# Kernel optimization log

Measured on AMD Instinct MI355X. Metric: run time of the kernel, lower is better.

The kernel has to match this reference:

```python
import jax, jax.numpy as jnp
import numpy as np

B, N, E = 8, 50000, 400000
DIMS = [4, 64, 64, 3]
K = 3
EPS = 1e-5
NEG_SLOPE = 0.01


def _gcn_norm(edge_index, num_nodes):
    # TAGConv uses gcn_norm with unit edge weights and add_self_loops=False.
    row, col = edge_index[0], edge_index[1]
    w = jnp.ones(row.shape[0], dtype=jnp.float32)
    deg = jax.ops.segment_sum(w, col, num_segments=num_nodes)  # in-degree at target
    dis = jnp.where(deg > 0, jnp.power(jnp.maximum(deg, 1.0), -0.5), 0.0)
    return dis[row] * dis[col]  # [E]


def _tag_conv(x, W, b, row, col, norm, num_nodes):
    # x: [B, N, Fin]; W: [K+1, Fin, Fout]; b: [Fout]
    out = jnp.einsum('bnf,fg->bng', x, W[0])
    h = x
    for k in range(1, W.shape[0]):
        msg = h[:, row, :] * norm[None, :, None]            # [B, E, Fin] gather
        h = jnp.zeros((x.shape[0], num_nodes, x.shape[2]), x.dtype).at[:, col, :].add(msg)  # scatter-add
        out = out + jnp.einsum('bnf,fg->bng', h, W[k])
    return out + b


def _batchnorm(x2d, gamma, beta):
    # training-mode BatchNorm1d over batch dim (biased variance, eps=1e-5)
    mean = jnp.mean(x2d, axis=0)
    var = jnp.mean(jnp.square(x2d - mean), axis=0)
    return gamma * (x2d - mean) * jax.lax.rsqrt(var + EPS) + beta


def _leaky_relu(x):
    return jnp.where(x >= 0, x, NEG_SLOPE * x)


def setup_inputs() -> dict:
    key = jax.random.key(0)
    ks = jax.random.split(key, 12)
    inp = {}
    inp['x'] = jax.random.normal(ks[0], (B, N, DIMS[0]), dtype=jnp.float32)
    inp['edge_index'] = jax.random.randint(ks[1], (2, E), 0, N, dtype=jnp.int64)
    inp['val_min'] = jax.random.uniform(ks[2], (N, 3), dtype=jnp.float32) - 1.5
    inp['val_max'] = jax.random.uniform(ks[3], (N, 3), dtype=jnp.float32) + 0.5
    for l in range(3):
        fin, fout = DIMS[l], DIMS[l + 1]
        scale = 1.0 / np.sqrt(fin)
        inp[f'W{l}'] = jax.random.uniform(ks[4 + l], (K + 1, fin, fout), minval=-scale, maxval=scale, dtype=jnp.float32)
        inp[f'b{l}'] = jnp.zeros((fout,), jnp.float32)
    for l in range(2):
        inp[f'gamma{l}'] = jnp.ones((N * DIMS[l + 1],), jnp.float32)
        inp[f'beta{l}'] = jnp.zeros((N * DIMS[l + 1],), jnp.float32)
    return inp


def reference(x, edge_index, val_min, val_max, W0, b0, W1, b1, W2, b2,
              gamma0, beta0, gamma1, beta1):
    row, col = edge_index[0], edge_index[1]
    norm = _gcn_norm(edge_index, N)
    Ws = [W0, W1, W2]
    bs = [b0, b1, b2]
    gammas = [gamma0, gamma1]
    betas = [beta0, beta1]
    out = x
    for layer in range(2):  # num_layers - 1 hidden layers
        out = _tag_conv(out, Ws[layer], bs[layer], row, col, norm, N)
        d = DIMS[layer + 1]
        out = _batchnorm(out.reshape(-1, N * d), gammas[layer], betas[layer]).reshape(-1, N, d)
        out = _leaky_relu(out)
    out = _tag_conv(out, Ws[2], bs[2], row, col, norm, N)  # [B, N, 3]
    # non_linearity: gamma = min + (max - min) / (1 + exp(U))
    return val_min[None] + (val_max - val_min)[None] / (1.0 + jnp.exp(out))
```

## Files before the change

kernel.cpp:

```cpp
#include <hip/hip_runtime.h>
#include <math.h>

constexpr int B = 8;
constexpr int N = 50000;
constexpr int E = 400000;
constexpr float BN_EPS = 1e-5f;
constexpr float NEG = 0.01f;


__device__ __forceinline__ unsigned clamp_src(int s) {
    unsigned u = (unsigned)s;
    return (u < (unsigned)N) ? u : 0u;
}

__device__ __forceinline__ unsigned pack_bf16(float a, float b) {
    unsigned ua = __float_as_uint(a);
    unsigned ub = __float_as_uint(b);
    ua = (ua + 0x7FFFu + ((ua >> 16) & 1u)) >> 16;
    ub = (ub + 0x7FFFu + ((ub >> 16) & 1u)) >> 16;
    return (ub << 16) | (ua & 0xFFFFu);
}
__device__ __forceinline__ float unpack_lo(unsigned u) { return __uint_as_float(u << 16); }
__device__ __forceinline__ float unpack_hi(unsigned u) { return __uint_as_float(u & 0xFFFF0000u); }

__device__ __forceinline__ void store_row64_f32(float* p, const float acc[64]) {
#pragma unroll
    for (int q = 0; q < 16; ++q)
        *(float4*)(p + q * 4) = make_float4(acc[q * 4], acc[q * 4 + 1], acc[q * 4 + 2], acc[q * 4 + 3]);
}
__device__ __forceinline__ void store_row64_bf(void* op, const float acc[64]) {
    uint4* p = (uint4*)op;
#pragma unroll
    for (int q = 0; q < 8; ++q) {
        uint4 v;
        v.x = pack_bf16(acc[q * 8 + 0], acc[q * 8 + 1]);
        v.y = pack_bf16(acc[q * 8 + 2], acc[q * 8 + 3]);
        v.z = pack_bf16(acc[q * 8 + 4], acc[q * 8 + 5]);
        v.w = pack_bf16(acc[q * 8 + 6], acc[q * 8 + 7]);
        p[q] = v;
    }
}


__global__ __launch_bounds__(256) void deg_kernel(const int* __restrict__ col, float* __restrict__ deg) {
    int e = blockIdx.x * blockDim.x + threadIdx.x;
    if (e < E) atomicAdd(&deg[clamp_src(col[e])], 1.0f);
}

__global__ __launch_bounds__(256) void scan1_kernel(const float* __restrict__ deg,
                                                    int* __restrict__ part, int* __restrict__ bsum) {
    __shared__ int sm[4];
    int i = blockIdx.x * blockDim.x + threadIdx.x;
    int v = (i < N) ? (int)deg[i] : 0;
    int lane = threadIdx.x & 63, wv = threadIdx.x >> 6;
    int x = v;
#pragma unroll
    for (int off = 1; off < 64; off <<= 1) {
        int t = __shfl_up(x, off);
        if (lane >= off) x += t;
    }
    if (lane == 63) sm[wv] = x;
    __syncthreads();
    int add = 0;
#pragma unroll
    for (int w = 0; w < 4; ++w) if (w < wv) add += sm[w];
    if (i < N) part[i] = x - v + add;
    if (threadIdx.x == blockDim.x - 1) bsum[blockIdx.x] = x + add;
}

__global__ __launch_bounds__(256) void scan2_kernel(const int* __restrict__ bsum, int* __restrict__ boff,
                                                    int nb, int* __restrict__ rowptr) {
    __shared__ int sm[4];
    int i = threadIdx.x;
    int v = (i < nb) ? bsum[i] : 0;
    int lane = i & 63, wv = i >> 6;
    int x = v;
#pragma unroll
    for (int off = 1; off < 64; off <<= 1) {
        int t = __shfl_up(x, off);
        if (lane >= off) x += t;
    }
    if (lane == 63) sm[wv] = x;
    __syncthreads();
    int add = 0;
#pragma unroll
    for (int w = 0; w < 4; ++w) if (w < wv) add += sm[w];
    if (i < nb) boff[i] = x - v + add;
    if (i == 0) rowptr[N] = E;
}

__global__ __launch_bounds__(256) void scan3_kernel(const int* __restrict__ part, const int* __restrict__ boff,
                                                    int* __restrict__ rowptr) {
    int i = blockIdx.x * blockDim.x + threadIdx.x;
    if (i < N) rowptr[i] = part[i] + boff[blockIdx.x];
}

__global__ __launch_bounds__(256) void fill_kernel(const int* __restrict__ row, const int* __restrict__ col,
                                                   const float* __restrict__ deg, const int* __restrict__ rowptr,
                                                   int* __restrict__ cursor, int* __restrict__ csr_src,
                                                   float* __restrict__ csr_w) {
    int e = blockIdx.x * blockDim.x + threadIdx.x;
    if (e >= E) return;
    unsigned r = clamp_src(row[e]), c = clamp_src(col[e]);
    float dr = deg[r], dc = deg[c];
    float w = (dr > 0.f ? rsqrtf(dr) : 0.f) * (dc > 0.f ? rsqrtf(dc) : 0.f);
    unsigned p = (unsigned)(rowptr[c] + atomicAdd(&cursor[c], 1));
    if (p >= (unsigned)E) p = E - 1;
    csr_src[p] = (int)r;
    csr_w[p] = w;
}


template<bool INBF>
__global__ __launch_bounds__(256) void xprop_kernel(const void* __restrict__ xin, const int* __restrict__ rowptr,
                                                    const int* __restrict__ csr_src, const float* __restrict__ csr_w,
                                                    uint2* __restrict__ xout) {
    int b = blockIdx.x & 7;
    int nb = blockIdx.x >> 3;
    int n = nb * blockDim.x + threadIdx.x;
    if (n >= N) return;
    float a0 = 0.f, a1 = 0.f, a2 = 0.f, a3 = 0.f;
    int beg = rowptr[n], end = rowptr[n + 1];
    if (beg < 0) beg = 0;
    if (end > E) end = E;
    for (int i = beg; i < end; ++i) {
        unsigned s = clamp_src(csr_src[i]);
        float w = csr_w[i];
        if constexpr (!INBF) {
            float4 v = *((const float4*)xin + (size_t)b * N + s);
            a0 = fmaf(w, v.x, a0); a1 = fmaf(w, v.y, a1);
            a2 = fmaf(w, v.z, a2); a3 = fmaf(w, v.w, a3);
        } else {
            uint2 v = *((const uint2*)xin + (size_t)b * N + s);
            a0 = fmaf(w, unpack_lo(v.x), a0); a1 = fmaf(w, unpack_hi(v.x), a1);
            a2 = fmaf(w, unpack_lo(v.y), a2); a3 = fmaf(w, unpack_hi(v.y), a3);
        }
    }
    uint2 o;
    o.x = pack_bf16(a0, a1);
    o.y = pack_bf16(a2, a3);
    xout[(size_t)b * N + n] = o;
}


__global__ __launch_bounds__(256) void fused0_kernel(const float* __restrict__ x0, const uint2* __restrict__ x1,
                                                     const uint2* __restrict__ x2, const uint2* __restrict__ x3,
                                                     const float* __restrict__ W0, const float* __restrict__ bias,
                                                     const float* __restrict__ gamma, const float* __restrict__ beta,
                                                     void* __restrict__ h1) {
    int gid = blockIdx.x * blockDim.x + threadIdx.x;
    int wave = gid >> 6, lane = gid & 63;
    int n = wave * 8 + (lane >> 3);
    int b = lane & 7;
    if (n >= N) return;
    size_t ro = (size_t)b * N + n;
    float xv[16];
    {
        float4 v = *((const float4*)x0 + ro);
        xv[0] = v.x; xv[1] = v.y; xv[2] = v.z; xv[3] = v.w;
        uint2 u1 = x1[ro], u2 = x2[ro], u3 = x3[ro];
        xv[4] = unpack_lo(u1.x); xv[5] = unpack_hi(u1.x); xv[6] = unpack_lo(u1.y); xv[7] = unpack_hi(u1.y);
        xv[8] = unpack_lo(u2.x); xv[9] = unpack_hi(u2.x); xv[10] = unpack_lo(u2.y); xv[11] = unpack_hi(u2.y);
        xv[12] = unpack_lo(u3.x); xv[13] = unpack_hi(u3.x); xv[14] = unpack_lo(u3.y); xv[15] = unpack_hi(u3.y);
    }
    float acc[64];
#pragma unroll
    for (int f = 0; f < 64; ++f) acc[f] = bias[f];
#pragma unroll
    for (int kf = 0; kf < 16; ++kf) {
        float xs = xv[kf];
#pragma unroll
        for (int f = 0; f < 64; ++f)
            acc[f] = fmaf(xs, W0[kf * 64 + f], acc[f]);
    }
    const float* gp = gamma + (size_t)n * 64;
    const float* bp = beta + (size_t)n * 64;
#pragma unroll
    for (int f = 0; f < 64; ++f) {
        float v = acc[f];
        float s = v, s2 = v * v;
        s += __shfl_xor(s, 1);  s += __shfl_xor(s, 2);  s += __shfl_xor(s, 4);
        s2 += __shfl_xor(s2, 1); s2 += __shfl_xor(s2, 2); s2 += __shfl_xor(s2, 4);
        float mean = s * 0.125f;
        float var = fmaf(-mean, mean, s2 * 0.125f);
        float xn = (v - mean) * rsqrtf(var + BN_EPS);
        float o = fmaf(gp[f], xn, bp[f]);
        acc[f] = (o >= 0.f) ? o : NEG * o;
    }
    store_row64_bf((char*)h1 + ro * 128, acc);
}


__device__ __forceinline__ void dense64_bf(const uint4* __restrict__ hp8, const float* __restrict__ W, float acc[64]) {
#pragma unroll 1
    for (int kk = 0; kk < 4; ++kk) {
        float hreg[16];
        uint4 va = hp8[kk * 2], vb = hp8[kk * 2 + 1];
        hreg[0] = unpack_lo(va.x); hreg[1] = unpack_hi(va.x);
        hreg[2] = unpack_lo(va.y); hreg[3] = unpack_hi(va.y);
        hreg[4] = unpack_lo(va.z); hreg[5] = unpack_hi(va.z);
        hreg[6] = unpack_lo(va.w); hreg[7] = unpack_hi(va.w);
        hreg[8] = unpack_lo(vb.x); hreg[9] = unpack_hi(vb.x);
        hreg[10] = unpack_lo(vb.y); hreg[11] = unpack_hi(vb.y);
        hreg[12] = unpack_lo(vb.z); hreg[13] = unpack_hi(vb.z);
        hreg[14] = unpack_lo(vb.w); hreg[15] = unpack_hi(vb.w);
        const float* Wp = W + kk * 16 * 64;
#pragma unroll
        for (int k = 0; k < 16; ++k) {
            float hv = hreg[k];
#pragma unroll
            for (int c = 0; c < 64; ++c)
                acc[c] = fmaf(hv, Wp[k * 64 + c], acc[c]);
        }
    }
}

__device__ __forceinline__ void gather64_f32(const float* __restrict__ ub, int beg, int end,
                                             const int* __restrict__ csr_src, const float* __restrict__ csr_w,
                                             float acc[64]) {
    if (beg < 0) beg = 0;
    if (end > E) end = E;
    for (int i = beg; i < end; ++i) {
        unsigned s = clamp_src(csr_src[i]);
        float w = csr_w[i];
        const float4* up = (const float4*)(ub + (size_t)s * 64);
#pragma unroll
        for (int q = 0; q < 16; ++q) {
            float4 v = up[q];
            acc[q * 4 + 0] = fmaf(w, v.x, acc[q * 4 + 0]);
            acc[q * 4 + 1] = fmaf(w, v.y, acc[q * 4 + 1]);
            acc[q * 4 + 2] = fmaf(w, v.z, acc[q * 4 + 2]);
            acc[q * 4 + 3] = fmaf(w, v.w, acc[q * 4 + 3]);
        }
    }
}

__device__ __forceinline__ void gather64_bf(const char* __restrict__ ub, int beg, int end,
                                            const int* __restrict__ csr_src, const float* __restrict__ csr_w,
                                            float acc[64]) {
    if (beg < 0) beg = 0;
    if (end > E) end = E;
    for (int i = beg; i < end; ++i) {
        unsigned s = clamp_src(csr_src[i]);
        float w = csr_w[i];
        const uint4* up = (const uint4*)(ub + (size_t)s * 128);
#pragma unroll
        for (int q = 0; q < 8; ++q) {
            uint4 v = up[q];
            acc[q * 8 + 0] = fmaf(w, unpack_lo(v.x), acc[q * 8 + 0]);
            acc[q * 8 + 1] = fmaf(w, unpack_hi(v.x), acc[q * 8 + 1]);
            acc[q * 8 + 2] = fmaf(w, unpack_lo(v.y), acc[q * 8 + 2]);
            acc[q * 8 + 3] = fmaf(w, unpack_hi(v.y), acc[q * 8 + 3]);
            acc[q * 8 + 4] = fmaf(w, unpack_lo(v.z), acc[q * 8 + 4]);
            acc[q * 8 + 5] = fmaf(w, unpack_hi(v.z), acc[q * 8 + 5]);
            acc[q * 8 + 6] = fmaf(w, unpack_lo(v.w), acc[q * 8 + 6]);
            acc[q * 8 + 7] = fmaf(w, unpack_hi(v.w), acc[q * 8 + 7]);
        }
    }
}


template<bool OUTBF>
__global__ __launch_bounds__(64) void hop_kernel(const float* __restrict__ u_in, const int* __restrict__ rowptr,
                                                 const int* __restrict__ csr_src, const float* __restrict__ csr_w,
                                                 const uint4* __restrict__ h1, int b0, int bshift, int bmask,
                                                 const float* __restrict__ W, void* __restrict__ out) {
    int bl = blockIdx.x & bmask;
    int n = (blockIdx.x >> bshift) * blockDim.x + threadIdx.x;
    if (n >= N) return;
    int gb = b0 + bl;
    float acc[64];
#pragma unroll
    for (int f = 0; f < 64; ++f) acc[f] = 0.f;
    if (u_in)
        gather64_f32(u_in + (size_t)bl * N * 64, rowptr[n], rowptr[n + 1], csr_src, csr_w, acc);
    dense64_bf(h1 + ((size_t)gb * N + n) * 8, W, acc);
    if constexpr (OUTBF)
        store_row64_bf((char*)out + ((size_t)gb * N + n) * 128, acc);
    else
        store_row64_f32((float*)out + ((size_t)bl * N + n) * 64, acc);
}


template<bool UBF>
__global__ __launch_bounds__(256) void hop64_final_kernel(const void* __restrict__ u_in, const int* __restrict__ rowptr,
                                                          const int* __restrict__ csr_src, const float* __restrict__ csr_w,
                                                          const uint4* __restrict__ h1, const float* __restrict__ W,
                                                          const float* __restrict__ bias,
                                                          const float* __restrict__ gamma, const float* __restrict__ beta,
                                                          const float* __restrict__ W2, float* __restrict__ y) {
    int gid = blockIdx.x * blockDim.x + threadIdx.x;
    int wave = gid >> 6, lane = gid & 63;
    int n = wave * 8 + (lane >> 3);
    int b = lane & 7;
    if (n >= N) return;
    float acc[64];
#pragma unroll
    for (int f = 0; f < 64; ++f) acc[f] = bias[f];
    int beg = rowptr[n], end = rowptr[n + 1];
    if constexpr (UBF)
        gather64_bf((const char*)u_in + (size_t)b * N * 128, beg, end, csr_src, csr_w, acc);
    else
        gather64_f32((const float*)u_in + (size_t)b * N * 64, beg, end, csr_src, csr_w, acc);
    dense64_bf(h1 + ((size_t)b * N + n) * 8, W, acc);
    const float* gp = gamma + (size_t)n * 64;
    const float* bp = beta + (size_t)n * 64;
#pragma unroll
    for (int f = 0; f < 64; ++f) {
        float v = acc[f];
        float s = v, s2 = v * v;
        s += __shfl_xor(s, 1);  s += __shfl_xor(s, 2);  s += __shfl_xor(s, 4);
        s2 += __shfl_xor(s2, 1); s2 += __shfl_xor(s2, 2); s2 += __shfl_xor(s2, 4);
        float mean = s * 0.125f;
        float var = fmaf(-mean, mean, s2 * 0.125f);
        float xn = (v - mean) * rsqrtf(var + BN_EPS);
        float o = fmaf(gp[f], xn, bp[f]);
        acc[f] = (o >= 0.f) ? o : NEG * o;
    }
    size_t bn3 = ((size_t)b * N + n) * 3;
#pragma unroll
    for (int k = 0; k < 4; ++k) {
#pragma unroll
        for (int c = 0; c < 3; ++c) {
            float s = 0.f;
#pragma unroll
            for (int f = 0; f < 64; ++f)
                s = fmaf(acc[f], W2[k * 192 + f * 3 + c], s);
            y[(size_t)k * B * N * 3 + bn3 + c] = s;
        }
    }
}


__global__ __launch_bounds__(256) void qprop_kernel(const float* __restrict__ vin, const int* __restrict__ rowptr,
                                                    const int* __restrict__ csr_src, const float* __restrict__ csr_w,
                                                    const float* __restrict__ add, float* __restrict__ vout) {
    int b = blockIdx.x & 7;
    int nb = blockIdx.x >> 3;
    int n = nb * blockDim.x + threadIdx.x;
    if (n >= N) return;
    float a0 = 0.f, a1 = 0.f, a2 = 0.f;
    int beg = rowptr[n], end = rowptr[n + 1];
    if (beg < 0) beg = 0;
    if (end > E) end = E;
    const float* base = vin + (size_t)b * N * 3;
    for (int i = beg; i < end; ++i) {
        unsigned s = clamp_src(csr_src[i]);
        float w = csr_w[i];
        const float* p = base + (size_t)s * 3;
        a0 = fmaf(w, p[0], a0);
        a1 = fmaf(w, p[1], a1);
        a2 = fmaf(w, p[2], a2);
    }
    const float* ap = add + ((size_t)b * N + n) * 3;
    float* op = vout + ((size_t)b * N + n) * 3;
    op[0] = a0 + ap[0];
    op[1] = a1 + ap[1];
    op[2] = a2 + ap[2];
}

__global__ __launch_bounds__(256) void qfinal_kernel(const float* __restrict__ vin, const int* __restrict__ rowptr,
                                                     const int* __restrict__ csr_src, const float* __restrict__ csr_w,
                                                     const float* __restrict__ y0, const float* __restrict__ b2,
                                                     const float* __restrict__ vmin, const float* __restrict__ vmax,
                                                     float* __restrict__ out) {
    int b = blockIdx.x & 7;
    int nb = blockIdx.x >> 3;
    int n = nb * blockDim.x + threadIdx.x;
    if (n >= N) return;
    float a0 = 0.f, a1 = 0.f, a2 = 0.f;
    int beg = rowptr[n], end = rowptr[n + 1];
    if (beg < 0) beg = 0;
    if (end > E) end = E;
    const float* base = vin + (size_t)b * N * 3;
    for (int i = beg; i < end; ++i) {
        unsigned s = clamp_src(csr_src[i]);
        float w = csr_w[i];
        const float* p = base + (size_t)s * 3;
        a0 = fmaf(w, p[0], a0);
        a1 = fmaf(w, p[1], a1);
        a2 = fmaf(w, p[2], a2);
    }
    size_t bn3 = ((size_t)b * N + n) * 3;
    const float* yp = y0 + bn3;
    float g0 = a0 + yp[0] + b2[0];
    float g1 = a1 + yp[1] + b2[1];
    float g2 = a2 + yp[2] + b2[2];
    float mn0 = vmin[n * 3 + 0], mx0 = vmax[n * 3 + 0];
    float mn1 = vmin[n * 3 + 1], mx1 = vmax[n * 3 + 1];
    float mn2 = vmin[n * 3 + 2], mx2 = vmax[n * 3 + 2];
    float* op = out + bn3;
    op[0] = mn0 + (mx0 - mn0) / (1.f + expf(g0));
    op[1] = mn1 + (mx1 - mn1) / (1.f + expf(g1));
    op[2] = mn2 + (mx2 - mn2) / (1.f + expf(g2));
}


extern "C" void kernel_launch(void* const* d_in, const int* in_sizes, int n_in,
                              void* d_out, int out_size, void* d_ws, size_t ws_size,
                              hipStream_t stream) {
    const float* x      = (const float*)d_in[0];
    const int*   ei     = (const int*)d_in[1];
    const int*   rowi   = ei;
    const int*   coli   = ei + E;
    const float* vmin   = (const float*)d_in[2];
    const float* vmax   = (const float*)d_in[3];
    const float* W0     = (const float*)d_in[4];
    const float* b0v    = (const float*)d_in[5];
    const float* W1     = (const float*)d_in[6];
    const float* b1v    = (const float*)d_in[7];
    const float* W2     = (const float*)d_in[8];
    const float* b2v    = (const float*)d_in[9];
    const float* gamma0 = (const float*)d_in[10];
    const float* beta0  = (const float*)d_in[11];
    const float* gamma1 = (const float*)d_in[12];
    const float* beta1  = (const float*)d_in[13];
    float* out = (float*)d_out;

    const size_t PC   = (size_t)N * 64;
    const size_t BN3  = (size_t)B * N * 3;
    const size_t H1FL = (size_t)B * N * 32;
    const size_t XBFL = (size_t)B * N * 2;
    const size_t avail_fl = ws_size / 4;

    auto rnd = [](size_t nf) { return (nf + 63) & ~(size_t)63; };
    const size_t csr_fl = rnd(N) + rnd(E) + rnd(N + 1) + rnd(N) + 256 + 256 + rnd(N) + rnd(E);

    int cc;
    size_t yv_fl = rnd(4 * BN3) + 2 * rnd(BN3);
    auto shared_need = [&](int c) { return (size_t)2 * c * PC > yv_fl ? (size_t)2 * c * PC : yv_fl; };
    auto tot_chunked = [&](int c) { return csr_fl + H1FL + H1FL + shared_need(c); };
    size_t tot_full = csr_fl + H1FL + 2 * 8 * PC;
    if (avail_fl >= tot_full + (1 << 20))      cc = 8;
    else if (avail_fl >= tot_chunked(4) + (1 << 20)) cc = 4;
    else if (avail_fl >= tot_chunked(2) + (1 << 20)) cc = 2;
    else cc = 1;

    size_t off = 0;
    auto alloc = [&](size_t nfloats) -> float* {
        float* p = (float*)d_ws + off;
        off += rnd(nfloats);
        return p;
    };
    float* deg     = alloc(N);
    float* csr_w   = alloc(E);
    int*   rowptr  = (int*)alloc(N + 1);
    int*   part    = (int*)alloc(N);
    int*   bsum    = (int*)alloc(256);
    int*   boff    = (int*)alloc(256);
    int*   cursor  = (int*)alloc(N);
    int*   csr_src = (int*)alloc(E);
    float* h1      = alloc(H1FL);

    float *u_a, *u_b, *u2full = nullptr, *shared;
    uint2 *xb1, *xb2, *xb3;
    float *y, *v_a, *v_b;
    if (cc == 8) {
        u_a = alloc(8 * PC);
        u_b = alloc(8 * PC);
        xb1 = (uint2*)u_b; xb2 = (uint2*)(u_b + XBFL); xb3 = (uint2*)(u_b + 2 * XBFL);
        y = u_b; v_a = u_b + rnd(4 * BN3); v_b = v_a + rnd(BN3);
    } else {
        u2full = alloc(H1FL);
        shared = alloc(shared_need(cc));
        u_a = shared; u_b = shared + (size_t)cc * PC;
        xb1 = (uint2*)shared; xb2 = (uint2*)(shared + XBFL); xb3 = (uint2*)(shared + 2 * XBFL);
        y = shared; v_a = shared + rnd(4 * BN3); v_b = v_a + rnd(BN3);
    }

    const int GE = (E + 255) / 256;
    const int GN = (N + 255) / 256;
    const int GT = (B * N + 255) / 256;
    const int GH = (N + 63) / 64;
    dim3 blk(256);
    int bshift = (cc == 8) ? 3 : (cc == 4) ? 2 : (cc == 2) ? 1 : 0;
    int bmask = cc - 1;

    hipMemsetAsync(deg, 0, N * sizeof(float), stream);
    hipMemsetAsync(cursor, 0, N * sizeof(int), stream);
    deg_kernel<<<GE, blk, 0, stream>>>(coli, deg);
    scan1_kernel<<<GN, blk, 0, stream>>>(deg, part, bsum);
    scan2_kernel<<<1, blk, 0, stream>>>(bsum, boff, GN, rowptr);
    scan3_kernel<<<GN, blk, 0, stream>>>(part, boff, rowptr);
    fill_kernel<<<GE, blk, 0, stream>>>(rowi, coli, deg, rowptr, cursor, csr_src, csr_w);

    xprop_kernel<false><<<GN * 8, blk, 0, stream>>>(x,   rowptr, csr_src, csr_w, xb1);
    xprop_kernel<true><<<GN * 8, blk, 0, stream>>>(xb1, rowptr, csr_src, csr_w, xb2);
    xprop_kernel<true><<<GN * 8, blk, 0, stream>>>(xb2, rowptr, csr_src, csr_w, xb3);
    fused0_kernel<<<GT, blk, 0, stream>>>(x, xb1, xb2, xb3, W0, b0v, gamma0, beta0, h1);

    if (cc == 8) {
        hop_kernel<false><<<GH * 8, dim3(64), 0, stream>>>(nullptr, rowptr, csr_src, csr_w,
                                                           (const uint4*)h1, 0, 3, 7, W1 + 3 * 4096, u_a);
        hop_kernel<false><<<GH * 8, dim3(64), 0, stream>>>(u_a, rowptr, csr_src, csr_w,
                                                           (const uint4*)h1, 0, 3, 7, W1 + 2 * 4096, u_b);
        hop_kernel<false><<<GH * 8, dim3(64), 0, stream>>>(u_b, rowptr, csr_src, csr_w,
                                                           (const uint4*)h1, 0, 3, 7, W1 + 1 * 4096, u_a);
        hop64_final_kernel<false><<<GT, blk, 0, stream>>>(u_a, rowptr, csr_src, csr_w,
                                                          (const uint4*)h1, W1, b1v, gamma1, beta1, W2, y);
    } else {
        for (int b0 = 0; b0 < B; b0 += cc) {
            hop_kernel<false><<<GH * cc, dim3(64), 0, stream>>>(nullptr, rowptr, csr_src, csr_w,
                                                                (const uint4*)h1, b0, bshift, bmask,
                                                                W1 + 3 * 4096, u_a);
            hop_kernel<false><<<GH * cc, dim3(64), 0, stream>>>(u_a, rowptr, csr_src, csr_w,
                                                                (const uint4*)h1, b0, bshift, bmask,
                                                                W1 + 2 * 4096, u_b);
            hop_kernel<true><<<GH * cc, dim3(64), 0, stream>>>(u_b, rowptr, csr_src, csr_w,
                                                               (const uint4*)h1, b0, bshift, bmask,
                                                               W1 + 1 * 4096, u2full);
        }
        hop64_final_kernel<true><<<GT, blk, 0, stream>>>(u2full, rowptr, csr_src, csr_w,
                                                         (const uint4*)h1, W1, b1v, gamma1, beta1, W2, y);
    }

    qprop_kernel<<<GN * 8, blk, 0, stream>>>(y + 3 * BN3, rowptr, csr_src, csr_w, y + 2 * BN3, v_a);
    qprop_kernel<<<GN * 8, blk, 0, stream>>>(v_a, rowptr, csr_src, csr_w, y + 1 * BN3, v_b);
    qfinal_kernel<<<GN * 8, blk, 0, stream>>>(v_b, rowptr, csr_src, csr_w, y, b2v, vmin, vmax, out);
}
```

Measured before the change: 1.105 ms.

## Recompute layer-0 activations inside hop kernels instead of materializing h1

Layer 0 is split into a stats kernel that stores per-feature BatchNorm scale and shift (packed bf16) and no longer writes h1. Each layer-1 hop kernel recomputes h1 on the fly from the propagated inputs, W0 and the scale/shift, and then applies Wk. Hop intermediates become bf16 with 256-thread blocks, and the chunked memory-fallback paths are removed. This trades extra ALU work (a 16x64 recompute in each of four hops) for less memory traffic and bf16 gathers. Dropping b0 from the pre-BatchNorm value is exact, since training-mode BN removes the mean. Storing u in bf16 and scale/shift in bf16 lowers precision.

```diff
diff --git a/kernel.cpp b/kernel.cpp
--- a/kernel.cpp
+++ b/kernel.cpp
@@ -23,13 +23,7 @@
 __device__ __forceinline__ float unpack_lo(unsigned u) { return __uint_as_float(u << 16); }
 __device__ __forceinline__ float unpack_hi(unsigned u) { return __uint_as_float(u & 0xFFFF0000u); }
 
-__device__ __forceinline__ void store_row64_f32(float* p, const float acc[64]) {
-#pragma unroll
-    for (int q = 0; q < 16; ++q)
-        *(float4*)(p + q * 4) = make_float4(acc[q * 4], acc[q * 4 + 1], acc[q * 4 + 2], acc[q * 4 + 3]);
-}
-__device__ __forceinline__ void store_row64_bf(void* op, const float acc[64]) {
-    uint4* p = (uint4*)op;
+__device__ __forceinline__ void store_row64_bf(uint4* p, const float acc[64]) {
 #pragma unroll
     for (int q = 0; q < 8; ++q) {
         uint4 v;
@@ -116,8 +110,7 @@
                                                     const int* __restrict__ csr_src, const float* __restrict__ csr_w,
                                                     uint2* __restrict__ xout) {
     int b = blockIdx.x & 7;
-    int nb = blockIdx.x >> 3;
-    int n = nb * blockDim.x + threadIdx.x;
+    int n = (blockIdx.x >> 3) * blockDim.x + threadIdx.x;
     if (n >= N) return;
     float a0 = 0.f, a1 = 0.f, a2 = 0.f, a3 = 0.f;
     int beg = rowptr[n], end = rowptr[n + 1];
@@ -143,11 +136,23 @@
 }
 
 
-__global__ __launch_bounds__(256) void fused0_kernel(const float* __restrict__ x0, const uint2* __restrict__ x1,
-                                                     const uint2* __restrict__ x2, const uint2* __restrict__ x3,
-                                                     const float* __restrict__ W0, const float* __restrict__ bias,
-                                                     const float* __restrict__ gamma, const float* __restrict__ beta,
-                                                     void* __restrict__ h1) {
+__device__ __forceinline__ void load_xv(const float4* __restrict__ x0, const uint2* __restrict__ x1,
+                                        const uint2* __restrict__ x2, const uint2* __restrict__ x3,
+                                        size_t ro, float xv[16]) {
+    float4 v = x0[ro];
+    xv[0] = v.x; xv[1] = v.y; xv[2] = v.z; xv[3] = v.w;
+    uint2 u1 = x1[ro], u2 = x2[ro], u3 = x3[ro];
+    xv[4] = unpack_lo(u1.x); xv[5] = unpack_hi(u1.x); xv[6] = unpack_lo(u1.y); xv[7] = unpack_hi(u1.y);
+    xv[8] = unpack_lo(u2.x); xv[9] = unpack_hi(u2.x); xv[10] = unpack_lo(u2.y); xv[11] = unpack_hi(u2.y);
+    xv[12] = unpack_lo(u3.x); xv[13] = unpack_hi(u3.x); xv[14] = unpack_lo(u3.y); xv[15] = unpack_hi(u3.y);
+}
+
+
+__global__ __launch_bounds__(256) void stats_kernel(const float4* __restrict__ x0, const uint2* __restrict__ x1,
+                                                    const uint2* __restrict__ x2, const uint2* __restrict__ x3,
+                                                    const float* __restrict__ W0,
+                                                    const float* __restrict__ gamma, const float* __restrict__ beta,
+                                                    unsigned* __restrict__ ss) {
     int gid = blockIdx.x * blockDim.x + threadIdx.x;
     int wave = gid >> 6, lane = gid & 63;
     int n = wave * 8 + (lane >> 3);
@@ -155,87 +160,36 @@
     if (n >= N) return;
     size_t ro = (size_t)b * N + n;
     float xv[16];
-    {
-        float4 v = *((const float4*)x0 + ro);
-        xv[0] = v.x; xv[1] = v.y; xv[2] = v.z; xv[3] = v.w;
-        uint2 u1 = x1[ro], u2 = x2[ro], u3 = x3[ro];
-        xv[4] = unpack_lo(u1.x); xv[5] = unpack_hi(u1.x); xv[6] = unpack_lo(u1.y); xv[7] = unpack_hi(u1.y);
-        xv[8] = unpack_lo(u2.x); xv[9] = unpack_hi(u2.x); xv[10] = unpack_lo(u2.y); xv[11] = unpack_hi(u2.y);
-        xv[12] = unpack_lo(u3.x); xv[13] = unpack_hi(u3.x); xv[14] = unpack_lo(u3.y); xv[15] = unpack_hi(u3.y);
-    }
-    float acc[64];
-#pragma unroll
-    for (int f = 0; f < 64; ++f) acc[f] = bias[f];
+    load_xv(x0, x1, x2, x3, ro, xv);
+    float z[64];
+#pragma unroll
+    for (int f = 0; f < 64; ++f) z[f] = 0.f;
 #pragma unroll
     for (int kf = 0; kf < 16; ++kf) {
         float xs = xv[kf];
 #pragma unroll
         for (int f = 0; f < 64; ++f)
-            acc[f] = fmaf(xs, W0[kf * 64 + f], acc[f]);
+            z[f] = fmaf(xs, W0[kf * 64 + f], z[f]);
     }
     const float* gp = gamma + (size_t)n * 64;
     const float* bp = beta + (size_t)n * 64;
 #pragma unroll
     for (int f = 0; f < 64; ++f) {
-        float v = acc[f];
+        float v = z[f];
         float s = v, s2 = v * v;
         s += __shfl_xor(s, 1);  s += __shfl_xor(s, 2);  s += __shfl_xor(s, 4);
         s2 += __shfl_xor(s2, 1); s2 += __shfl_xor(s2, 2); s2 += __shfl_xor(s2, 4);
         float mean = s * 0.125f;
         float var = fmaf(-mean, mean, s2 * 0.125f);
-        float xn = (v - mean) * rsqrtf(var + BN_EPS);
-        float o = fmaf(gp[f], xn, bp[f]);
-        acc[f] = (o >= 0.f) ? o : NEG * o;
-    }
-    store_row64_bf((char*)h1 + ro * 128, acc);
-}
-
-
-__device__ __forceinline__ void dense64_bf(const uint4* __restrict__ hp8, const float* __restrict__ W, float acc[64]) {
-#pragma unroll 1
-    for (int kk = 0; kk < 4; ++kk) {
-        float hreg[16];
-        uint4 va = hp8[kk * 2], vb = hp8[kk * 2 + 1];
-        hreg[0] = unpack_lo(va.x); hreg[1] = unpack_hi(va.x);
-        hreg[2] = unpack_lo(va.y); hreg[3] = unpack_hi(va.y);
-        hreg[4] = unpack_lo(va.z); hreg[5] = unpack_hi(va.z);
-        hreg[6] = unpack_lo(va.w); hreg[7] = unpack_hi(va.w);
-        hreg[8] = unpack_lo(vb.x); hreg[9] = unpack_hi(vb.x);
-        hreg[10] = unpack_lo(vb.y); hreg[11] = unpack_hi(vb.y);
-        hreg[12] = unpack_lo(vb.z); hreg[13] = unpack_hi(vb.z);
-        hreg[14] = unpack_lo(vb.w); hreg[15] = unpack_hi(vb.w);
-        const float* Wp = W + kk * 16 * 64;
-#pragma unroll
-        for (int k = 0; k < 16; ++k) {
-            float hv = hreg[k];
-#pragma unroll
-            for (int c = 0; c < 64; ++c)
-                acc[c] = fmaf(hv, Wp[k * 64 + c], acc[c]);
-        }
-    }
-}
-
-__device__ __forceinline__ void gather64_f32(const float* __restrict__ ub, int beg, int end,
-                                             const int* __restrict__ csr_src, const float* __restrict__ csr_w,
-                                             float acc[64]) {
-    if (beg < 0) beg = 0;
-    if (end > E) end = E;
-    for (int i = beg; i < end; ++i) {
-        unsigned s = clamp_src(csr_src[i]);
-        float w = csr_w[i];
-        const float4* up = (const float4*)(ub + (size_t)s * 64);
-#pragma unroll
-        for (int q = 0; q < 16; ++q) {
-            float4 v = up[q];
-            acc[q * 4 + 0] = fmaf(w, v.x, acc[q * 4 + 0]);
-            acc[q * 4 + 1] = fmaf(w, v.y, acc[q * 4 + 1]);
-            acc[q * 4 + 2] = fmaf(w, v.z, acc[q * 4 + 2]);
-            acc[q * 4 + 3] = fmaf(w, v.w, acc[q * 4 + 3]);
-        }
-    }
-}
-
-__device__ __forceinline__ void gather64_bf(const char* __restrict__ ub, int beg, int end,
+        float rs = rsqrtf(var + BN_EPS);
+        float sc = gp[f] * rs;
+        float sh = fmaf(-sc, mean, bp[f]);
+        if (b == 0) ss[(size_t)n * 64 + f] = pack_bf16(sc, sh);
+    }
+}
+
+
+__device__ __forceinline__ void gather64_bf(const uint4* __restrict__ ub8, int beg, int end,
                                             const int* __restrict__ csr_src, const float* __restrict__ csr_w,
                                             float acc[64]) {
     if (beg < 0) beg = 0;
@@ -243,7 +197,7 @@
     for (int i = beg; i < end; ++i) {
         unsigned s = clamp_src(csr_src[i]);
         float w = csr_w[i];
-        const uint4* up = (const uint4*)(ub + (size_t)s * 128);
+        const uint4* up = ub8 + (size_t)s * 8;
 #pragma unroll
         for (int q = 0; q < 8; ++q) {
             uint4 v = up[q];
@@ -260,49 +214,72 @@
 }
 
 
-template<bool OUTBF>
-__global__ __launch_bounds__(64) void hop_kernel(const float* __restrict__ u_in, const int* __restrict__ rowptr,
-                                                 const int* __restrict__ csr_src, const float* __restrict__ csr_w,
-                                                 const uint4* __restrict__ h1, int b0, int bshift, int bmask,
-                                                 const float* __restrict__ W, void* __restrict__ out) {
-    int bl = blockIdx.x & bmask;
-    int n = (blockIdx.x >> bshift) * blockDim.x + threadIdx.x;
-    if (n >= N) return;
-    int gb = b0 + bl;
+template<int MODE>
+__global__ __launch_bounds__(256) void hopR_kernel(const uint4* __restrict__ u_in, const int* __restrict__ rowptr,
+                                                   const int* __restrict__ csr_src, const float* __restrict__ csr_w,
+                                                   const float4* __restrict__ x0, const uint2* __restrict__ x1,
+                                                   const uint2* __restrict__ x2, const uint2* __restrict__ x3,
+                                                   const float* __restrict__ W0, const unsigned* __restrict__ ss,
+                                                   const float* __restrict__ Wk, const float* __restrict__ bias,
+                                                   uint4* __restrict__ u_out) {
+    int b = blockIdx.x & 7;
+    int n = (blockIdx.x >> 3) * blockDim.x + threadIdx.x;
+    if (n >= N) return;
+    size_t ro = (size_t)b * N + n;
+    float xv[16];
+    load_xv(x0, x1, x2, x3, ro, xv);
     float acc[64];
-#pragma unroll
-    for (int f = 0; f < 64; ++f) acc[f] = 0.f;
-    if (u_in)
-        gather64_f32(u_in + (size_t)bl * N * 64, rowptr[n], rowptr[n + 1], csr_src, csr_w, acc);
-    dense64_bf(h1 + ((size_t)gb * N + n) * 8, W, acc);
-    if constexpr (OUTBF)
-        store_row64_bf((char*)out + ((size_t)gb * N + n) * 128, acc);
-    else
-        store_row64_f32((float*)out + ((size_t)bl * N + n) * 64, acc);
-}
-
-
-template<bool UBF>
-__global__ __launch_bounds__(256) void hop64_final_kernel(const void* __restrict__ u_in, const int* __restrict__ rowptr,
-                                                          const int* __restrict__ csr_src, const float* __restrict__ csr_w,
-                                                          const uint4* __restrict__ h1, const float* __restrict__ W,
-                                                          const float* __restrict__ bias,
-                                                          const float* __restrict__ gamma, const float* __restrict__ beta,
-                                                          const float* __restrict__ W2, float* __restrict__ y) {
+    if constexpr (MODE == 2) {
+#pragma unroll
+        for (int f = 0; f < 64; ++f) acc[f] = bias[f];
+    } else {
+#pragma unroll
+        for (int f = 0; f < 64; ++f) acc[f] = 0.f;
+    }
+    if constexpr (MODE > 0)
+        gather64_bf(u_in + (size_t)b * N * 8, rowptr[n], rowptr[n + 1], csr_src, csr_w, acc);
+    const unsigned* ssp = ss + (size_t)n * 64;
+#pragma unroll 1
+    for (int kq = 0; kq < 16; ++kq) {
+        uint4 sq = *(const uint4*)(ssp + kq * 4);
+        unsigned sqa[4] = {sq.x, sq.y, sq.z, sq.w};
+#pragma unroll
+        for (int j = 0; j < 4; ++j) {
+            int k = kq * 4 + j;
+            float z = 0.f;
+#pragma unroll
+            for (int kf = 0; kf < 16; ++kf)
+                z = fmaf(xv[kf], W0[kf * 64 + k], z);
+            float h = fmaf(z, unpack_lo(sqa[j]), unpack_hi(sqa[j]));
+            h = (h >= 0.f) ? h : NEG * h;
+            const float* wr = Wk + k * 64;
+#pragma unroll
+            for (int c = 0; c < 64; ++c)
+                acc[c] = fmaf(h, wr[c], acc[c]);
+        }
+    }
+    store_row64_bf(u_out + ro * 8, acc);
+}
+
+
+__global__ __launch_bounds__(256) void bn_project_kernel(const uint4* __restrict__ z,
+                                                         const float* __restrict__ gamma, const float* __restrict__ beta,
+                                                         const float* __restrict__ W2, float* __restrict__ y) {
     int gid = blockIdx.x * blockDim.x + threadIdx.x;
     int wave = gid >> 6, lane = gid & 63;
     int n = wave * 8 + (lane >> 3);
     int b = lane & 7;
     if (n >= N) return;
     float acc[64];
-#pragma unroll
-    for (int f = 0; f < 64; ++f) acc[f] = bias[f];
-    int beg = rowptr[n], end = rowptr[n + 1];
-    if constexpr (UBF)
-        gather64_bf((const char*)u_in + (size_t)b * N * 128, beg, end, csr_src, csr_w, acc);
-    else
-        gather64_f32((const float*)u_in + (size_t)b * N * 64, beg, end, csr_src, csr_w, acc);
-    dense64_bf(h1 + ((size_t)b * N + n) * 8, W, acc);
+    const uint4* zp = z + ((size_t)b * N + n) * 8;
+#pragma unroll
+    for (int q = 0; q < 8; ++q) {
+        uint4 v = zp[q];
+        acc[q * 8 + 0] = unpack_lo(v.x); acc[q * 8 + 1] = unpack_hi(v.x);
+        acc[q * 8 + 2] = unpack_lo(v.y); acc[q * 8 + 3] = unpack_hi(v.y);
+        acc[q * 8 + 4] = unpack_lo(v.z); acc[q * 8 + 5] = unpack_hi(v.z);
+        acc[q * 8 + 6] = unpack_lo(v.w); acc[q * 8 + 7] = unpack_hi(v.w);
+    }
     const float* gp = gamma + (size_t)n * 64;
     const float* bp = beta + (size_t)n * 64;
 #pragma unroll
@@ -336,8 +313,7 @@
                                                     const int* __restrict__ csr_src, const float* __restrict__ csr_w,
                                                     const float* __restrict__ add, float* __restrict__ vout) {
     int b = blockIdx.x & 7;
-    int nb = blockIdx.x >> 3;
-    int n = nb * blockDim.x + threadIdx.x;
+    int n = (blockIdx.x >> 3) * blockDim.x + threadIdx.x;
     if (n >= N) return;
     float a0 = 0.f, a1 = 0.f, a2 = 0.f;
     int beg = rowptr[n], end = rowptr[n + 1];
@@ -365,8 +341,7 @@
                                                      const float* __restrict__ vmin, const float* __restrict__ vmax,
                                                      float* __restrict__ out) {
     int b = blockIdx.x & 7;
-    int nb = blockIdx.x >> 3;
-    int n = nb * blockDim.x + threadIdx.x;
+    int n = (blockIdx.x >> 3) * blockDim.x + threadIdx.x;
     if (n >= N) return;
     float a0 = 0.f, a1 = 0.f, a2 = 0.f;
     int beg = rowptr[n], end = rowptr[n + 1];
@@ -406,7 +381,6 @@
     const float* vmin   = (const float*)d_in[2];
     const float* vmax   = (const float*)d_in[3];
     const float* W0     = (const float*)d_in[4];
-    const float* b0v    = (const float*)d_in[5];
     const float* W1     = (const float*)d_in[6];
     const float* b1v    = (const float*)d_in[7];
     const float* W2     = (const float*)d_in[8];
@@ -417,25 +391,11 @@
     const float* beta1  = (const float*)d_in[13];
     float* out = (float*)d_out;
 
-    const size_t PC   = (size_t)N * 64;
     const size_t BN3  = (size_t)B * N * 3;
-    const size_t H1FL = (size_t)B * N * 32;
+    const size_t UFL  = (size_t)B * N * 32;
     const size_t XBFL = (size_t)B * N * 2;
-    const size_t avail_fl = ws_size / 4;
 
     auto rnd = [](size_t nf) { return (nf + 63) & ~(size_t)63; };
-    const size_t csr_fl = rnd(N) + rnd(E) + rnd(N + 1) + rnd(N) + 256 + 256 + rnd(N) + rnd(E);
-
-    int cc;
-    size_t yv_fl = rnd(4 * BN3) + 2 * rnd(BN3);
-    auto shared_need = [&](int c) { return (size_t)2 * c * PC > yv_fl ? (size_t)2 * c * PC : yv_fl; };
-    auto tot_chunked = [&](int c) { return csr_fl + H1FL + H1FL + shared_need(c); };
-    size_t tot_full = csr_fl + H1FL + 2 * 8 * PC;
-    if (avail_fl >= tot_full + (1 << 20))      cc = 8;
-    else if (avail_fl >= tot_chunked(4) + (1 << 20)) cc = 4;
-    else if (avail_fl >= tot_chunked(2) + (1 << 20)) cc = 2;
-    else cc = 1;
-
     size_t off = 0;
     auto alloc = [&](size_t nfloats) -> float* {
         float* p = (float*)d_ws + off;
@@ -450,31 +410,21 @@
     int*   boff    = (int*)alloc(256);
     int*   cursor  = (int*)alloc(N);
     int*   csr_src = (int*)alloc(E);
-    float* h1      = alloc(H1FL);
-
-    float *u_a, *u_b, *u2full = nullptr, *shared;
-    uint2 *xb1, *xb2, *xb3;
-    float *y, *v_a, *v_b;
-    if (cc == 8) {
-        u_a = alloc(8 * PC);
-        u_b = alloc(8 * PC);
-        xb1 = (uint2*)u_b; xb2 = (uint2*)(u_b + XBFL); xb3 = (uint2*)(u_b + 2 * XBFL);
-        y = u_b; v_a = u_b + rnd(4 * BN3); v_b = v_a + rnd(BN3);
-    } else {
-        u2full = alloc(H1FL);
-        shared = alloc(shared_need(cc));
-        u_a = shared; u_b = shared + (size_t)cc * PC;
-        xb1 = (uint2*)shared; xb2 = (uint2*)(shared + XBFL); xb3 = (uint2*)(shared + 2 * XBFL);
-        y = shared; v_a = shared + rnd(4 * BN3); v_b = v_a + rnd(BN3);
-    }
-
-    const int GE = (E + 255) / 256;
-    const int GN = (N + 255) / 256;
-    const int GT = (B * N + 255) / 256;
-    const int GH = (N + 63) / 64;
+    uint2* xb1     = (uint2*)alloc(XBFL);
+    uint2* xb2     = (uint2*)alloc(XBFL);
+    uint2* xb3     = (uint2*)alloc(XBFL);
+    unsigned* ss   = (unsigned*)alloc((size_t)N * 64);
+    float* u_a     = alloc(UFL);
+    float* u_b     = alloc(UFL);
+    float* y   = u_a;
+    float* v_a = u_a + rnd(4 * BN3);
+    float* v_b = v_a + rnd(BN3);
+
+    const int GE  = (E + 255) / 256;
+    const int GN  = (N + 255) / 256;
+    const int GT  = (B * N + 255) / 256;
+    const int GB8 = GN * 8;
     dim3 blk(256);
-    int bshift = (cc == 8) ? 3 : (cc == 4) ? 2 : (cc == 2) ? 1 : 0;
-    int bmask = cc - 1;
 
     hipMemsetAsync(deg, 0, N * sizeof(float), stream);
     hipMemsetAsync(cursor, 0, N * sizeof(int), stream);
@@ -484,37 +434,26 @@
     scan3_kernel<<<GN, blk, 0, stream>>>(part, boff, rowptr);
     fill_kernel<<<GE, blk, 0, stream>>>(rowi, coli, deg, rowptr, cursor, csr_src, csr_w);
 
-    xprop_kernel<false><<<GN * 8, blk, 0, stream>>>(x,   rowptr, csr_src, csr_w, xb1);
-    xprop_kernel<true><<<GN * 8, blk, 0, stream>>>(xb1, rowptr, csr_src, csr_w, xb2);
-    xprop_kernel<true><<<GN * 8, blk, 0, stream>>>(xb2, rowptr, csr_src, csr_w, xb3);
-    fused0_kernel<<<GT, blk, 0, stream>>>(x, xb1, xb2, xb3, W0, b0v, gamma0, beta0, h1);
-
-    if (cc == 8) {
-        hop_kernel<false><<<GH * 8, dim3(64), 0, stream>>>(nullptr, rowptr, csr_src, csr_w,
-                                                           (const uint4*)h1, 0, 3, 7, W1 + 3 * 4096, u_a);
-        hop_kernel<false><<<GH * 8, dim3(64), 0, stream>>>(u_a, rowptr, csr_src, csr_w,
-                                                           (const uint4*)h1, 0, 3, 7, W1 + 2 * 4096, u_b);
-        hop_kernel<false><<<GH * 8, dim3(64), 0, stream>>>(u_b, rowptr, csr_src, csr_w,
-                                                           (const uint4*)h1, 0, 3, 7, W1 + 1 * 4096, u_a);
-        hop64_final_kernel<false><<<GT, blk, 0, stream>>>(u_a, rowptr, csr_src, csr_w,
-                                                          (const uint4*)h1, W1, b1v, gamma1, beta1, W2, y);
-    } else {
-        for (int b0 = 0; b0 < B; b0 += cc) {
-            hop_kernel<false><<<GH * cc, dim3(64), 0, stream>>>(nullptr, rowptr, csr_src, csr_w,
-                                                                (const uint4*)h1, b0, bshift, bmask,
-                                                                W1 + 3 * 4096, u_a);
-            hop_kernel<false><<<GH * cc, dim3(64), 0, stream>>>(u_a, rowptr, csr_src, csr_w,
-                                                                (const uint4*)h1, b0, bshift, bmask,
-                                                                W1 + 2 * 4096, u_b);
-            hop_kernel<true><<<GH * cc, dim3(64), 0, stream>>>(u_b, rowptr, csr_src, csr_w,
-                                                               (const uint4*)h1, b0, bshift, bmask,
-                                                               W1 + 1 * 4096, u2full);
-        }
-        hop64_final_kernel<true><<<GT, blk, 0, stream>>>(u2full, rowptr, csr_src, csr_w,
-                                                         (const uint4*)h1, W1, b1v, gamma1, beta1, W2, y);
-    }
-
-    qprop_kernel<<<GN * 8, blk, 0, stream>>>(y + 3 * BN3, rowptr, csr_src, csr_w, y + 2 * BN3, v_a);
-    qprop_kernel<<<GN * 8, blk, 0, stream>>>(v_a, rowptr, csr_src, csr_w, y + 1 * BN3, v_b);
-    qfinal_kernel<<<GN * 8, blk, 0, stream>>>(v_b, rowptr, csr_src, csr_w, y, b2v, vmin, vmax, out);
-}
+    xprop_kernel<false><<<GB8, blk, 0, stream>>>(x,   rowptr, csr_src, csr_w, xb1);
+    xprop_kernel<true><<<GB8, blk, 0, stream>>>(xb1, rowptr, csr_src, csr_w, xb2);
+    xprop_kernel<true><<<GB8, blk, 0, stream>>>(xb2, rowptr, csr_src, csr_w, xb3);
+    stats_kernel<<<GT, blk, 0, stream>>>((const float4*)x, xb1, xb2, xb3, W0, gamma0, beta0, ss);
+
+    hopR_kernel<0><<<GB8, blk, 0, stream>>>(nullptr, rowptr, csr_src, csr_w,
+                                            (const float4*)x, xb1, xb2, xb3, W0, ss,
+                                            W1 + 3 * 4096, nullptr, (uint4*)u_a);
+    hopR_kernel<1><<<GB8, blk, 0, stream>>>((const uint4*)u_a, rowptr, csr_src, csr_w,
+                                            (const float4*)x, xb1, xb2, xb3, W0, ss,
+                                            W1 + 2 * 4096, nullptr, (uint4*)u_b);
+    hopR_kernel<1><<<GB8, blk, 0, stream>>>((const uint4*)u_b, rowptr, csr_src, csr_w,
+                                            (const float4*)x, xb1, xb2, xb3, W0, ss,
+                                            W1 + 1 * 4096, nullptr, (uint4*)u_a);
+    hopR_kernel<2><<<GB8, blk, 0, stream>>>((const uint4*)u_a, rowptr, csr_src, csr_w,
+                                            (const float4*)x, xb1, xb2, xb3, W0, ss,
+                                            W1, b1v, (uint4*)u_b);
+    bn_project_kernel<<<GT, blk, 0, stream>>>((const uint4*)u_b, gamma1, beta1, W2, y);
+
+    qprop_kernel<<<GB8, blk, 0, stream>>>(y + 3 * BN3, rowptr, csr_src, csr_w, y + 2 * BN3, v_a);
+    qprop_kernel<<<GB8, blk, 0, stream>>>(v_a, rowptr, csr_src, csr_w, y + 1 * BN3, v_b);
+    qfinal_kernel<<<GB8, blk, 0, stream>>>(v_b, rowptr, csr_src, csr_w, y, b2v, vmin, vmax, out);
+}
```

New measurement: 1.090 ms. About the same (-1.3%).
